# Optimization experiments

Measured on AMD Instinct MI355X. Metric: run time of the kernel, lower is better.

Reference implementation:

```python
import jax, jax.numpy as jnp
import numpy as np

B, S, DIM = 2, 2048, 2048
H = 16
Q_RANK, KV_RANK = 512, 512
D_NOPE, D_ROPE, D_V = 128, 64, 128
D_QK = D_NOPE + D_ROPE  # 192
EPS = 1e-6
SCALE = D_QK ** -0.5


def setup_inputs() -> dict:
    key = jax.random.key(0)
    ks = jax.random.split(key, 8)
    x = jax.random.normal(ks[0], (B, S, DIM), dtype=jnp.float32)
    # real RoPE table: theta_i = 10000^{-2i/d}, angles = pos * theta
    inv_freq = 1.0 / (10000.0 ** (np.arange(0, D_ROPE, 2, dtype=np.float32) / D_ROPE))
    ang = np.arange(S, dtype=np.float32)[:, None] * inv_freq[None, :]  # (S, D_ROPE//2)
    freqs_cis = jnp.asarray(np.stack([np.cos(ang), np.sin(ang)], axis=-1))  # (S, 32, 2)
    std = 0.02
    wq_a = jax.random.normal(ks[1], (Q_RANK, DIM), dtype=jnp.float32) * std
    wq_b = jax.random.normal(ks[2], (H * D_QK, Q_RANK), dtype=jnp.float32) * std
    wkv_a = jax.random.normal(ks[3], (KV_RANK + D_ROPE, DIM), dtype=jnp.float32) * std
    wkv_b = jax.random.normal(ks[4], (H * (D_NOPE + D_V), KV_RANK), dtype=jnp.float32) * std
    wo = jax.random.normal(ks[5], (DIM, H * D_V), dtype=jnp.float32) * std
    q_norm_w = jnp.ones((Q_RANK,), dtype=jnp.float32)
    kv_norm_w = jnp.ones((KV_RANK,), dtype=jnp.float32)
    return {"x": x, "freqs_cis": freqs_cis, "wq_a": wq_a, "wq_b": wq_b,
            "q_norm_w": q_norm_w, "wkv_a": wkv_a, "kv_norm_w": kv_norm_w,
            "wkv_b": wkv_b, "wo": wo}


def _rmsnorm(x, w):
    var = jnp.mean(jnp.square(x), axis=-1, keepdims=True)
    return x * jax.lax.rsqrt(var + EPS) * w


def _rope(x, freqs_cis):
    # x: (B, S, h, d); freqs_cis: (S, d//2, 2) as (cos, sin). Pairs are interleaved (x0,x1),(x2,x3),...
    xr, xi = x[..., 0::2], x[..., 1::2]
    cos = freqs_cis[None, :, None, :, 0]
    sin = freqs_cis[None, :, None, :, 1]
    yr = xr * cos - xi * sin
    yi = xr * sin + xi * cos
    return jnp.stack([yr, yi], axis=-1).reshape(x.shape)


def reference(x, freqs_cis, wq_a, wq_b, q_norm_w, wkv_a, kv_norm_w, wkv_b, wo):
    b, s, _ = x.shape
    # low-rank Q projection: wq_a -> RMSNorm -> wq_b
    q = _rmsnorm(x @ wq_a.T, q_norm_w) @ wq_b.T
    q = q.reshape(b, s, H, D_QK)
    q_nope, q_pe = q[..., :D_NOPE], q[..., D_NOPE:]
    q = jnp.concatenate([q_nope, _rope(q_pe, freqs_cis)], axis=-1)  # (b,s,H,192)
    # KV path
    kv = x @ wkv_a.T  # (b,s,KV_RANK+D_ROPE)
    kv_lat, k_pe = kv[..., :KV_RANK], kv[..., KV_RANK:]
    k_pe = _rope(k_pe[:, :, None, :], freqs_cis)  # (b,s,1,64)
    kv = (_rmsnorm(kv_lat, kv_norm_w) @ wkv_b.T).reshape(b, s, H, D_NOPE + D_V)
    k_nope, v = kv[..., :D_NOPE], kv[..., D_NOPE:]
    k = jnp.concatenate([k_nope, jnp.broadcast_to(k_pe, (b, s, H, D_ROPE))], axis=-1)
    # causal scaled-dot-product attention
    scores = jnp.einsum('bshd,bthd->bhst', q, k) * SCALE
    mask = jnp.tril(jnp.ones((s, s), dtype=bool))
    scores = jnp.where(mask[None, None], scores, jnp.finfo(scores.dtype).min)
    probs = jax.nn.softmax(scores, axis=-1)
    out = jnp.einsum('bhst,bthd->bshd', probs, v).reshape(b, s, H * D_V)
    return out @ wo.T
```

## Files before the change

### kernel.cpp

```cpp
#include <hip/hip_runtime.h>
#include <cstdint>
#include <cstddef>


typedef unsigned short u16;
typedef unsigned int u32;
typedef unsigned long long u64;
typedef __attribute__((ext_vector_type(8))) short bf16x8;
typedef __attribute__((ext_vector_type(4))) float floatx4;

#define MFMA16x16x32 __builtin_amdgcn_mfma_f32_16x16x32_bf16

#define QSCALE 0.10411755f
#define THR_L2 11.541560f

__device__ __forceinline__ u16 f2bf(float f) {
  u32 u = __float_as_uint(f);
  u32 r = (u + 0x7fffu + ((u >> 16) & 1u)) >> 16;
  return (u16)r;
}

__device__ __forceinline__ u32 cvtpk(float lo, float hi) {
  u32 r;
  asm("v_cvt_pk_bf16_f32 %0, %1, %2" : "=v"(r) : "v"(lo), "v"(hi));
  return r;
}

__device__ __forceinline__ void gload16(const void* g, void* l) {
  __builtin_amdgcn_global_load_lds(
      (const __attribute__((address_space(1))) void*)g,
      (__attribute__((address_space(3))) void*)l, 16, 0, 0);
}

__global__ __launch_bounds__(256) void cvt_all(
    const float* __restrict__ s0, const float* __restrict__ s1,
    const float* __restrict__ s2, const float* __restrict__ s3,
    const float* __restrict__ s4, const float* __restrict__ s5,
    u16* __restrict__ d0, u16* __restrict__ d1, u16* __restrict__ d2,
    u16* __restrict__ d3, u16* __restrict__ d4, u16* __restrict__ d5) {
  constexpr int ST1 = 2097152;
  constexpr int ST2 = ST1 + 262144;
  constexpr int ST3 = ST2 + 294912;
  constexpr int ST4 = ST3 + 393216;
  constexpr int ST5 = ST4 + 524288;
  constexpr int TOT = ST5 + 1048576;
  int i = blockIdx.x * 256 + threadIdx.x;
  int stride = gridDim.x * 256;
  for (; i < TOT; i += stride) {
    const float* sp;
    u16* dp;
    int j;
    if (i < ST1)      { sp = s0; dp = d0; j = i; }
    else if (i < ST2) { sp = s1; dp = d1; j = i - ST1; }
    else if (i < ST3) { sp = s2; dp = d2; j = i - ST2; }
    else if (i < ST4) { sp = s3; dp = d3; j = i - ST3; }
    else if (i < ST5) { sp = s4; dp = d4; j = i - ST4; }
    else              { sp = s5; dp = d5; j = i - ST5; }
    float4 v = ((const float4*)sp)[j];
    ushort4 o;
    o.x = f2bf(v.x); o.y = f2bf(v.y); o.z = f2bf(v.z); o.w = f2bf(v.w);
    ((ushort4*)dp)[j] = o;
  }
}

template <int BN>
__global__ __launch_bounds__(256) void gemm_bt(const u16* __restrict__ A,
                                               const u16* __restrict__ B,
                                               float* __restrict__ C,
                                               int M, int N, int K) {
  constexpr int FN = BN / 32;
  constexpr int BL = BN / 64;
  __shared__ alignas(16) u16 As[2][128 * 32];
  __shared__ alignas(16) u16 Bs[2][BN * 32];
  const int m0 = blockIdx.y * 128, n0 = blockIdx.x * BN;
  const int t = threadIdx.x;
  const int wv = t >> 6, lane = t & 63, g = lane >> 4, qq = lane & 15;
  const int wr = wv >> 1, wc = wv & 1;
  const int fsw = (qq >> 1) & 3;
  size_t aoff[2], boff[BL];
#pragma unroll
  for (int i = 0; i < 2; ++i) {
    int seg = t + i * 256;
    int row = seg >> 2, sl = seg & 3;
    aoff[i] = (size_t)(m0 + row) * K + (sl ^ ((row >> 1) & 3)) * 8;
  }
#pragma unroll
  for (int i = 0; i < BL; ++i) {
    int seg = t + i * 256;
    int row = seg >> 2, sl = seg & 3;
    boff[i] = (size_t)(n0 + row) * K + (sl ^ ((row >> 1) & 3)) * 8;
  }
  const floatx4 fz = {0.f, 0.f, 0.f, 0.f};
  floatx4 acc[4][FN];
#pragma unroll
  for (int m = 0; m < 4; ++m)
#pragma unroll
    for (int n = 0; n < FN; ++n) acc[m][n] = fz;

#define GSTAGE(buf, k0)                                                      \
  {                                                                          \
    _Pragma("unroll") for (int i = 0; i < 2; ++i)                            \
        gload16(&A[aoff[i] + (k0)], &As[buf][(size_t)(wv * 64 + i * 256) * 8]); \
    _Pragma("unroll") for (int i = 0; i < BL; ++i)                           \
        gload16(&B[boff[i] + (k0)], &Bs[buf][(size_t)(wv * 64 + i * 256) * 8]); \
  }

  const int nk = K >> 5;
  GSTAGE(0, 0);
  for (int kt = 0; kt < nk; ++kt) {
    asm volatile("" ::: "memory");
    if (kt + 1 < nk) {
      GSTAGE((kt + 1) & 1, (kt + 1) * 32);
      if constexpr (BN == 128)
        asm volatile("s_waitcnt vmcnt(4)" ::: "memory");
      else
        asm volatile("s_waitcnt vmcnt(3)" ::: "memory");
    } else {
      asm volatile("s_waitcnt vmcnt(0)" ::: "memory");
    }
    __builtin_amdgcn_s_barrier();
    asm volatile("" ::: "memory");
    const u16* Ab = &As[kt & 1][0];
    const u16* Bb = &Bs[kt & 1][0];
    bf16x8 af[4], bfr[FN];
#pragma unroll
    for (int m = 0; m < 4; ++m)
      af[m] = *(const bf16x8*)&Ab[(wr * 64 + m * 16 + qq) * 32 + ((g ^ fsw) * 8)];
#pragma unroll
    for (int n = 0; n < FN; ++n)
      bfr[n] = *(const bf16x8*)&Bb[(wc * (BN / 2) + n * 16 + qq) * 32 + ((g ^ fsw) * 8)];
    __builtin_amdgcn_s_setprio(1);
#pragma unroll
    for (int m = 0; m < 4; ++m)
#pragma unroll
      for (int n = 0; n < FN; ++n)
        acc[m][n] = MFMA16x16x32(af[m], bfr[n], acc[m][n], 0, 0, 0);
    __builtin_amdgcn_s_setprio(0);
    asm volatile("" ::: "memory");
    __builtin_amdgcn_s_barrier();
  }
#undef GSTAGE
#pragma unroll
  for (int m = 0; m < 4; ++m)
#pragma unroll
    for (int n = 0; n < FN; ++n)
#pragma unroll
      for (int r = 0; r < 4; ++r) {
        int row = m0 + wr * 64 + m * 16 + 4 * g + r;
        int col = n0 + wc * (BN / 2) + n * 16 + qq;
        C[(size_t)row * N + col] = acc[m][n][r];
      }
}

__global__ __launch_bounds__(256) void rmsnorm_bf16(const float* __restrict__ in,
                                                    int stride,
                                                    const float* __restrict__ w,
                                                    u16* __restrict__ out) {
  const int row = blockIdx.x, t = threadIdx.x;
  __shared__ float wsum[4];
  float2 v = *(const float2*)&in[(size_t)row * stride + 2 * t];
  float ss = v.x * v.x + v.y * v.y;
#pragma unroll
  for (int off = 1; off < 64; off <<= 1) ss += __shfl_xor(ss, off);
  if ((t & 63) == 0) wsum[t >> 6] = ss;
  __syncthreads();
  float tot = wsum[0] + wsum[1] + wsum[2] + wsum[3];
  float r = rsqrtf(tot * (1.f / 512.f) + 1e-6f);
  out[(size_t)row * 512 + 2 * t] = f2bf(v.x * r * w[2 * t]);
  out[(size_t)row * 512 + 2 * t + 1] = f2bf(v.y * r * w[2 * t + 1]);
}

__global__ __launch_bounds__(256) void rope_kpe(const float* __restrict__ ap,
                                                const float* __restrict__ fc,
                                                u16* __restrict__ kpe) {
  int idx = blockIdx.x * 256 + threadIdx.x;
  int row = idx >> 5, j = idx & 31;
  int s = row & 2047;
  float xr = ap[(size_t)row * 1088 + 1024 + 2 * j];
  float xi = ap[(size_t)row * 1088 + 1024 + 2 * j + 1];
  float c = fc[(s * 32 + j) * 2], sn = fc[(s * 32 + j) * 2 + 1];
  u32 lo = f2bf(xr * c - xi * sn), hi = f2bf(xr * sn + xi * c);
  *(u32*)&kpe[(size_t)row * 64 + 2 * j] = lo | (hi << 16);
}

__global__ __launch_bounds__(256) void rope_pack_q(const float* __restrict__ qf,
                                                   const float* __restrict__ fc,
                                                   u16* __restrict__ qbf) {
  int idx = blockIdx.x * 256 + threadIdx.x;
  int j = idx % 96;
  int rh = idx / 96;
  int h = rh & 15, row = rh >> 4;
  int b = row >> 11, s = row & 2047;
  const float* src = qf + (size_t)row * 3072 + h * 192;
  u16* dst = qbf + ((size_t)(b * 16 + h) * 2048 + s) * 192;
  if (j < 64) {
    u32 lo = f2bf(src[2 * j] * QSCALE), hi = f2bf(src[2 * j + 1] * QSCALE);
    *(u32*)&dst[2 * j] = lo | (hi << 16);
  } else {
    int jp = j - 64;
    float xr = src[128 + 2 * jp], xi = src[128 + 2 * jp + 1];
    float c = fc[(s * 32 + jp) * 2], sn = fc[(s * 32 + jp) * 2 + 1];
    u32 lo = f2bf((xr * c - xi * sn) * QSCALE);
    u32 hi = f2bf((xr * sn + xi * c) * QSCALE);
    *(u32*)&dst[128 + 2 * jp] = lo | (hi << 16);
  }
}

__global__ __launch_bounds__(256) void pack_k(const float* __restrict__ kvb,
                                              const u16* __restrict__ kpe,
                                              u16* __restrict__ kbf) {
  int idx = blockIdx.x * 256 + threadIdx.x;
  int j = idx % 96;
  int rh = idx / 96;
  int h = rh & 15, row = rh >> 4;
  int b = row >> 11, s = row & 2047;
  u16* dst = kbf + ((size_t)(b * 16 + h) * 2048 + s) * 192;
  if (j < 64) {
    const float* src = kvb + (size_t)row * 4096 + h * 256;
    u32 lo = f2bf(src[2 * j]), hi = f2bf(src[2 * j + 1]);
    *(u32*)&dst[2 * j] = lo | (hi << 16);
  } else {
    int jp = j - 64;
    *(u32*)&dst[128 + 2 * jp] = *(const u32*)&kpe[(size_t)row * 64 + 2 * jp];
  }
}

__global__ __launch_bounds__(256) void transpose_v(const float* __restrict__ kvb,
                                                   u16* __restrict__ vt) {
  __shared__ u16 T[32][34];
  const int bh = blockIdx.z, b = bh >> 4, h = bh & 15;
  const int s0 = blockIdx.x * 32, d0 = blockIdx.y * 32;
  const int tx = threadIdx.x & 31, ty = threadIdx.x >> 5;
#pragma unroll
  for (int i = 0; i < 4; ++i) {
    int sl = ty + i * 8;
    float v = kvb[(size_t)(b * 2048 + s0 + sl) * 4096 + h * 256 + 128 + d0 + tx];
    T[sl][tx] = f2bf(v);
  }
  __syncthreads();
#pragma unroll
  for (int i = 0; i < 4; ++i) {
    int dl = ty + i * 8;
    vt[((size_t)bh * 128 + d0 + dl) * 2048 + s0 + tx] = T[tx][dl];
  }
}

__global__ __launch_bounds__(256, 4) void flash_attn(const u16* __restrict__ Q,
                                                     const u16* __restrict__ Kc,
                                                     const u16* __restrict__ VT,
                                                     u16* __restrict__ O) {
  __shared__ alignas(16) u16 Ks[2][32 * 192];
  __shared__ alignas(16) u16 Vs[2][128 * 32];
  const int bid = blockIdx.x;
  const int qt = 31 - (bid >> 5);
  const int bh = bid & 31;
  const int t = threadIdx.x, wv = t >> 6, lane = t & 63;
  const int g = lane >> 4, qq = lane & 15;
  const int qrow0 = qt * 64 + wv * 16;
  const int my_last = qrow0 + 15;
  const int q_glob = qrow0 + qq;
  const int nkt = 2 * qt + 2;

  int koffg[3], voffg[2];
#pragma unroll
  for (int i = 0; i < 3; ++i) {
    int seg = t + i * 256;
    int row = seg / 24, sl = seg - row * 24;
    koffg[i] = row * 192 + (sl ^ ((row >> 1) & 7)) * 8;
  }
#pragma unroll
  for (int i = 0; i < 2; ++i) {
    int seg = t + i * 256;
    int row = seg >> 2, sl = seg & 3;
    voffg[i] = row * 2048 + (sl ^ ((row >> 1) & 3)) * 8;
  }
  const u16* Kt0 = Kc + (size_t)bh * 2048 * 192;
  const u16* Vt0 = VT + (size_t)bh * 128 * 2048;

  bf16x8 qf[6];
  {
    const u16* qp = Q + ((size_t)bh * 2048 + qrow0 + qq) * 192;
#pragma unroll
    for (int kk = 0; kk < 6; ++kk) qf[kk] = *(const bf16x8*)&qp[kk * 32 + g * 8];
  }
  asm volatile("s_waitcnt vmcnt(0)" ::: "memory");

  const floatx4 fz = {0.f, 0.f, 0.f, 0.f};
  floatx4 oacc[8];
  floatx4 oacc_l = fz;
#pragma unroll
  for (int d = 0; d < 8; ++d) oacc[d] = fz;
  float m_run = -1e30f;

  bf16x8 ones;
#pragma unroll
  for (int i = 0; i < 8; ++i) ones[i] = (short)0x3f80;

  const int krow0 = 2 * qq;
  const int krow1 = 2 * qq + 1;
  const int xrk = qq & 7;
  const int vsw = (qq >> 1) & 3;

#define STAGE(buf, kt)                                                       \
  {                                                                          \
    const u16* Kg = Kt0 + (size_t)(kt) * (32 * 192);                         \
    const u16* Vg = Vt0 + (kt) * 32;                                         \
    _Pragma("unroll") for (int i = 0; i < 3; ++i)                            \
        gload16(Kg + koffg[i], &Ks[buf][(size_t)(wv * 64 + i * 256) * 8]);   \
    _Pragma("unroll") for (int i = 0; i < 2; ++i)                            \
        gload16(Vg + voffg[i], &Vs[buf][(size_t)(wv * 64 + i * 256) * 8]);   \
  }

  STAGE(0, 0);
  for (int kt = 0; kt < nkt; ++kt) {
    const int k0 = kt * 32;
    asm volatile("" ::: "memory");
    if (kt + 1 < nkt) {
      STAGE((kt + 1) & 1, kt + 1);
      asm volatile("s_waitcnt vmcnt(5)" ::: "memory");
    } else {
      asm volatile("s_waitcnt vmcnt(0)" ::: "memory");
    }
    __builtin_amdgcn_s_barrier();
    asm volatile("" ::: "memory");
    if (k0 <= my_last) {
      const u16* Kb = &Ks[kt & 1][0];
      const u16* Vb = &Vs[kt & 1][0];
      floatx4 s0 = fz, s1 = fz;
      __builtin_amdgcn_s_setprio(1);
#pragma unroll
      for (int kk = 0; kk < 6; ++kk) {
        int sl = kk * 4 + g;
        bf16x8 a0 = *(const bf16x8*)&Kb[krow0 * 192 + ((sl ^ xrk) * 8)];
        bf16x8 a1 = *(const bf16x8*)&Kb[krow1 * 192 + ((sl ^ xrk) * 8)];
        s0 = MFMA16x16x32(a0, qf[kk], s0, 0, 0, 0);
        s1 = MFMA16x16x32(a1, qf[kk], s1, 0, 0, 0);
      }
      __builtin_amdgcn_s_setprio(0);
      float v[8];
      if (k0 + 31 <= qrow0) {
#pragma unroll
        for (int r = 0; r < 4; ++r) {
          v[r] = s0[r];
          v[4 + r] = s1[r];
        }
      } else {
#pragma unroll
        for (int r = 0; r < 4; ++r) {
          int key0 = k0 + 8 * g + 2 * r;
          v[r] = (key0 <= q_glob) ? s0[r] : -1e30f;
          v[4 + r] = (key0 + 1 <= q_glob) ? s1[r] : -1e30f;
        }
      }
      float mloc = fmaxf(fmaxf(fmaxf(v[0], v[1]), fmaxf(v[2], v[3])),
                         fmaxf(fmaxf(v[4], v[5]), fmaxf(v[6], v[7])));
      if (!__all(mloc <= m_run + THR_L2)) {
        float mx = fmaxf(mloc, __shfl_xor(mloc, 16));
        mx = fmaxf(mx, __shfl_xor(mx, 32));
        float m_new = fmaxf(m_run, mx);
        float alpha = exp2f(m_run - m_new);
        m_run = m_new;
#pragma unroll
        for (int d = 0; d < 8; ++d)
#pragma unroll
          for (int r = 0; r < 4; ++r) oacc[d][r] *= alpha;
#pragma unroll
        for (int r = 0; r < 4; ++r) oacc_l[r] *= alpha;
      }
      float pex[8];
#pragma unroll
      for (int i = 0; i < 8; ++i) pex[i] = exp2f(v[i] - m_run);
      bf16x8 pf;
      ((u32*)&pf)[0] = cvtpk(pex[0], pex[4]);
      ((u32*)&pf)[1] = cvtpk(pex[1], pex[5]);
      ((u32*)&pf)[2] = cvtpk(pex[2], pex[6]);
      ((u32*)&pf)[3] = cvtpk(pex[3], pex[7]);
      __builtin_amdgcn_s_setprio(1);
#pragma unroll
      for (int d = 0; d < 8; ++d) {
        bf16x8 vf = *(const bf16x8*)&Vb[(d * 16 + qq) * 32 + ((g ^ vsw) * 8)];
        oacc[d] = MFMA16x16x32(vf, pf, oacc[d], 0, 0, 0);
      }
      oacc_l = MFMA16x16x32(ones, pf, oacc_l, 0, 0, 0);
      __builtin_amdgcn_s_setprio(0);
    }
    asm volatile("" ::: "memory");
    __builtin_amdgcn_s_barrier();
  }
#undef STAGE
  float linv = 1.f / oacc_l[0];
  const int b = bh >> 4, h = bh & 15;
  size_t rowoff = ((size_t)b * 2048 + qrow0 + qq) * 2048 + h * 128 + 4 * g;
#pragma unroll
  for (int d = 0; d < 8; ++d) {
    u32 lo = cvtpk(oacc[d][0] * linv, oacc[d][1] * linv);
    u32 hi = cvtpk(oacc[d][2] * linv, oacc[d][3] * linv);
    u64 w = (u64)lo | ((u64)hi << 32);
    *(u64*)&O[rowoff + d * 16] = w;
  }
}

extern "C" void kernel_launch(void* const* d_in, const int* in_sizes, int n_in,
                              void* d_out, int out_size, void* d_ws,
                              size_t ws_size, hipStream_t stream) {
  (void)in_sizes; (void)n_in; (void)out_size;
  const float* x = (const float*)d_in[0];
  const float* fc = (const float*)d_in[1];
  const float* wqa = (const float*)d_in[2];
  const float* wqb = (const float*)d_in[3];
  const float* qnw = (const float*)d_in[4];
  const float* wkva = (const float*)d_in[5];
  const float* kvnw = (const float*)d_in[6];
  const float* wkvb = (const float*)d_in[7];
  const float* wo = (const float*)d_in[8];
  float* out = (float*)d_out;
  char* ws = (char*)d_ws;

  size_t off = 0;
  auto alloc = [&](size_t bytes) {
    size_t o = off;
    off += (bytes + 255) & ~(size_t)255;
    return o;
  };
  const size_t o_xbf = alloc(16777216);
  const size_t o_wa = alloc(4456448);
  const size_t o_wqb = alloc(3145728);
  const size_t o_wkvb = alloc(4194304);
  const size_t o_wo = alloc(8388608);
  const size_t o_qln = alloc(4194304);
  const size_t o_kvln = alloc(4194304);
  const size_t o_kpe = alloc(524288);
  const size_t o_big = alloc(67108864);
  const size_t o_qbf = alloc(25165824);
  const size_t o_kbf = alloc(25165824);
  const size_t o_vt = alloc(16777216);
  if (ws_size < off) return;

  u16* xbf = (u16*)(ws + o_xbf);
  u16* wab = (u16*)(ws + o_wa);
  u16* wqbb = (u16*)(ws + o_wqb);
  u16* wkvbb = (u16*)(ws + o_wkvb);
  u16* wob = (u16*)(ws + o_wo);
  u16* qlatn = (u16*)(ws + o_qln);
  u16* kvlatn = (u16*)(ws + o_kvln);
  u16* kpe = (u16*)(ws + o_kpe);
  float* aproj = (float*)(ws + o_big);
  float* qfull = (float*)(ws + o_big);
  float* kvb = (float*)(ws + o_big);
  u16* qbf = (u16*)(ws + o_qbf);
  u16* kbf = (u16*)(ws + o_kbf);
  u16* vt = (u16*)(ws + o_vt);
  u16* attnbf = (u16*)(ws + o_xbf);

  cvt_all<<<2048, 256, 0, stream>>>(x, wqa, wkva, wqb, wkvb, wo,
                                    xbf, wab, wab + 1048576, wqbb, wkvbb, wob);

  gemm_bt<64><<<dim3(17, 32), 256, 0, stream>>>(xbf, wab, aproj, 4096, 1088, 2048);
  rmsnorm_bf16<<<4096, 256, 0, stream>>>(aproj, 1088, qnw, qlatn);
  rmsnorm_bf16<<<4096, 256, 0, stream>>>(aproj + 512, 1088, kvnw, kvlatn);
  rope_kpe<<<512, 256, 0, stream>>>(aproj, fc, kpe);

  gemm_bt<128><<<dim3(24, 32), 256, 0, stream>>>(qlatn, wqbb, qfull, 4096, 3072, 512);
  rope_pack_q<<<24576, 256, 0, stream>>>(qfull, fc, qbf);

  gemm_bt<128><<<dim3(32, 32), 256, 0, stream>>>(kvlatn, wkvbb, kvb, 4096, 4096, 512);
  pack_k<<<24576, 256, 0, stream>>>(kvb, kpe, kbf);
  transpose_v<<<dim3(64, 4, 32), 256, 0, stream>>>(kvb, vt);

  flash_attn<<<1024, 256, 0, stream>>>(qbf, kbf, vt, attnbf);
  gemm_bt<128><<<dim3(16, 32), 256, 0, stream>>>(attnbf, wob, out, 4096, 2048, 2048);
}
```

Measured before the change: 289.3 us.

## Replace GEMMs with 8-wave large-tile kernel and emit bf16 intermediates

Adds a templated 512-thread GEMM with 128x256 or 256x256 tiles. It keeps two K-stages in flight and reissues the next load right after the LDS fragment reads, instead of waiting for a trailing barrier. The Q and KV up-projection GEMMs now write bf16 directly, so the downstream rope, pack and transpose kernels read half the bytes and skip their own conversion. The first projection's N is padded from 1088 to 1280 to fit the tile. The padded weight rows are never written and the extra columns are wasted compute. The larger tiles give fewer blocks than there are CUs for some GEMMs.

```diff
diff --git a/kernel.cpp b/kernel.cpp
--- a/kernel.cpp
+++ b/kernel.cpp
@@ -19,13 +19,14 @@
   u32 r = (u + 0x7fffu + ((u >> 16) & 1u)) >> 16;
   return (u16)r;
 }
-
+__device__ __forceinline__ float bf2f(u16 b) {
+  return __uint_as_float(((u32)b) << 16);
+}
 __device__ __forceinline__ u32 cvtpk(float lo, float hi) {
   u32 r;
   asm("v_cvt_pk_bf16_f32 %0, %1, %2" : "=v"(r) : "v"(lo), "v"(hi));
   return r;
 }
-
 __device__ __forceinline__ void gload16(const void* g, void* l) {
   __builtin_amdgcn_global_load_lds(
       (const __attribute__((address_space(1))) void*)g,
@@ -63,55 +64,58 @@
   }
 }
 
-template <int BN>
-__global__ __launch_bounds__(256) void gemm_bt(const u16* __restrict__ A,
-                                               const u16* __restrict__ B,
-                                               float* __restrict__ C,
-                                               int M, int N, int K) {
-  constexpr int FN = BN / 32;
-  constexpr int BL = BN / 64;
-  __shared__ alignas(16) u16 As[2][128 * 32];
+template <int BM, int BN, bool OBF16>
+__global__ __launch_bounds__(512) void gemm8(const u16* __restrict__ A,
+                                             const u16* __restrict__ B,
+                                             void* __restrict__ Cv,
+                                             int M, int N, int K) {
+  constexpr int WM = BM / 2;
+  constexpr int AF = WM / 16;
+  constexpr int LA = BM * 4 / 512;
+  constexpr int LB = BN * 4 / 512;
+  constexpr int S = LA + LB;
+  __shared__ alignas(16) u16 As[2][BM * 32];
   __shared__ alignas(16) u16 Bs[2][BN * 32];
-  const int m0 = blockIdx.y * 128, n0 = blockIdx.x * BN;
+  const int m0 = blockIdx.y * BM, n0 = blockIdx.x * BN;
   const int t = threadIdx.x;
   const int wv = t >> 6, lane = t & 63, g = lane >> 4, qq = lane & 15;
-  const int wr = wv >> 1, wc = wv & 1;
+  const int wr = wv >> 2, wc = wv & 3;
   const int fsw = (qq >> 1) & 3;
-  size_t aoff[2], boff[BL];
-#pragma unroll
-  for (int i = 0; i < 2; ++i) {
-    int seg = t + i * 256;
+  size_t aoff[LA], boff[LB];
+#pragma unroll
+  for (int i = 0; i < LA; ++i) {
+    int seg = t + i * 512;
     int row = seg >> 2, sl = seg & 3;
     aoff[i] = (size_t)(m0 + row) * K + (sl ^ ((row >> 1) & 3)) * 8;
   }
 #pragma unroll
-  for (int i = 0; i < BL; ++i) {
-    int seg = t + i * 256;
+  for (int i = 0; i < LB; ++i) {
+    int seg = t + i * 512;
     int row = seg >> 2, sl = seg & 3;
     boff[i] = (size_t)(n0 + row) * K + (sl ^ ((row >> 1) & 3)) * 8;
   }
   const floatx4 fz = {0.f, 0.f, 0.f, 0.f};
-  floatx4 acc[4][FN];
-#pragma unroll
-  for (int m = 0; m < 4; ++m)
-#pragma unroll
-    for (int n = 0; n < FN; ++n) acc[m][n] = fz;
-
-#define GSTAGE(buf, k0)                                                      \
-  {                                                                          \
-    _Pragma("unroll") for (int i = 0; i < 2; ++i)                            \
-        gload16(&A[aoff[i] + (k0)], &As[buf][(size_t)(wv * 64 + i * 256) * 8]); \
-    _Pragma("unroll") for (int i = 0; i < BL; ++i)                           \
-        gload16(&B[boff[i] + (k0)], &Bs[buf][(size_t)(wv * 64 + i * 256) * 8]); \
+  floatx4 acc[AF][4];
+#pragma unroll
+  for (int m = 0; m < AF; ++m)
+#pragma unroll
+    for (int n = 0; n < 4; ++n) acc[m][n] = fz;
+
+#define GS8(buf, k0)                                                          \
+  {                                                                           \
+    _Pragma("unroll") for (int i = 0; i < LA; ++i)                            \
+        gload16(&A[aoff[i] + (k0)], &As[buf][(size_t)(wv * 64 + i * 512) * 8]); \
+    _Pragma("unroll") for (int i = 0; i < LB; ++i)                            \
+        gload16(&B[boff[i] + (k0)], &Bs[buf][(size_t)(wv * 64 + i * 512) * 8]); \
   }
 
   const int nk = K >> 5;
-  GSTAGE(0, 0);
+  GS8(0, 0);
+  GS8(1, 32);
   for (int kt = 0; kt < nk; ++kt) {
     asm volatile("" ::: "memory");
     if (kt + 1 < nk) {
-      GSTAGE((kt + 1) & 1, (kt + 1) * 32);
-      if constexpr (BN == 128)
+      if constexpr (S == 4)
         asm volatile("s_waitcnt vmcnt(4)" ::: "memory");
       else
         asm volatile("s_waitcnt vmcnt(3)" ::: "memory");
@@ -122,33 +126,38 @@
     asm volatile("" ::: "memory");
     const u16* Ab = &As[kt & 1][0];
     const u16* Bb = &Bs[kt & 1][0];
-    bf16x8 af[4], bfr[FN];
-#pragma unroll
-    for (int m = 0; m < 4; ++m)
-      af[m] = *(const bf16x8*)&Ab[(wr * 64 + m * 16 + qq) * 32 + ((g ^ fsw) * 8)];
-#pragma unroll
-    for (int n = 0; n < FN; ++n)
-      bfr[n] = *(const bf16x8*)&Bb[(wc * (BN / 2) + n * 16 + qq) * 32 + ((g ^ fsw) * 8)];
+    bf16x8 af[AF], bfr[4];
+#pragma unroll
+    for (int m = 0; m < AF; ++m)
+      af[m] = *(const bf16x8*)&Ab[(wr * WM + m * 16 + qq) * 32 + ((g ^ fsw) * 8)];
+#pragma unroll
+    for (int n = 0; n < 4; ++n)
+      bfr[n] = *(const bf16x8*)&Bb[(wc * 64 + n * 16 + qq) * 32 + ((g ^ fsw) * 8)];
+    asm volatile("s_waitcnt lgkmcnt(0)" ::: "memory");
+    __builtin_amdgcn_s_barrier();
+    asm volatile("" ::: "memory");
+    if (kt + 2 < nk) GS8(kt & 1, (kt + 2) * 32);
     __builtin_amdgcn_s_setprio(1);
 #pragma unroll
-    for (int m = 0; m < 4; ++m)
-#pragma unroll
-      for (int n = 0; n < FN; ++n)
+    for (int m = 0; m < AF; ++m)
+#pragma unroll
+      for (int n = 0; n < 4; ++n)
         acc[m][n] = MFMA16x16x32(af[m], bfr[n], acc[m][n], 0, 0, 0);
     __builtin_amdgcn_s_setprio(0);
-    asm volatile("" ::: "memory");
-    __builtin_amdgcn_s_barrier();
-  }
-#undef GSTAGE
-#pragma unroll
-  for (int m = 0; m < 4; ++m)
-#pragma unroll
-    for (int n = 0; n < FN; ++n)
+  }
+#undef GS8
+#pragma unroll
+  for (int m = 0; m < AF; ++m)
+#pragma unroll
+    for (int n = 0; n < 4; ++n)
 #pragma unroll
       for (int r = 0; r < 4; ++r) {
-        int row = m0 + wr * 64 + m * 16 + 4 * g + r;
-        int col = n0 + wc * (BN / 2) + n * 16 + qq;
-        C[(size_t)row * N + col] = acc[m][n][r];
+        int row = m0 + wr * WM + m * 16 + 4 * g + r;
+        int col = n0 + wc * 64 + n * 16 + qq;
+        if constexpr (OBF16)
+          ((u16*)Cv)[(size_t)row * N + col] = f2bf(acc[m][n][r]);
+        else
+          ((float*)Cv)[(size_t)row * N + col] = acc[m][n][r];
       }
 }
 
@@ -176,14 +185,14 @@
   int idx = blockIdx.x * 256 + threadIdx.x;
   int row = idx >> 5, j = idx & 31;
   int s = row & 2047;
-  float xr = ap[(size_t)row * 1088 + 1024 + 2 * j];
-  float xi = ap[(size_t)row * 1088 + 1024 + 2 * j + 1];
+  float xr = ap[(size_t)row * 1280 + 1024 + 2 * j];
+  float xi = ap[(size_t)row * 1280 + 1024 + 2 * j + 1];
   float c = fc[(s * 32 + j) * 2], sn = fc[(s * 32 + j) * 2 + 1];
   u32 lo = f2bf(xr * c - xi * sn), hi = f2bf(xr * sn + xi * c);
   *(u32*)&kpe[(size_t)row * 64 + 2 * j] = lo | (hi << 16);
 }
 
-__global__ __launch_bounds__(256) void rope_pack_q(const float* __restrict__ qf,
+__global__ __launch_bounds__(256) void rope_pack_q(const u16* __restrict__ qf,
                                                    const float* __restrict__ fc,
                                                    u16* __restrict__ qbf) {
   int idx = blockIdx.x * 256 + threadIdx.x;
@@ -191,14 +200,17 @@
   int rh = idx / 96;
   int h = rh & 15, row = rh >> 4;
   int b = row >> 11, s = row & 2047;
-  const float* src = qf + (size_t)row * 3072 + h * 192;
+  const u16* src = qf + (size_t)row * 3072 + h * 192;
   u16* dst = qbf + ((size_t)(b * 16 + h) * 2048 + s) * 192;
   if (j < 64) {
-    u32 lo = f2bf(src[2 * j] * QSCALE), hi = f2bf(src[2 * j + 1] * QSCALE);
+    u32 w = *(const u32*)&src[2 * j];
+    u32 lo = f2bf(bf2f((u16)w) * QSCALE);
+    u32 hi = f2bf(bf2f((u16)(w >> 16)) * QSCALE);
     *(u32*)&dst[2 * j] = lo | (hi << 16);
   } else {
     int jp = j - 64;
-    float xr = src[128 + 2 * jp], xi = src[128 + 2 * jp + 1];
+    u32 w = *(const u32*)&src[128 + 2 * jp];
+    float xr = bf2f((u16)w), xi = bf2f((u16)(w >> 16));
     float c = fc[(s * 32 + jp) * 2], sn = fc[(s * 32 + jp) * 2 + 1];
     u32 lo = f2bf((xr * c - xi * sn) * QSCALE);
     u32 hi = f2bf((xr * sn + xi * c) * QSCALE);
@@ -206,7 +218,7 @@
   }
 }
 
-__global__ __launch_bounds__(256) void pack_k(const float* __restrict__ kvb,
+__global__ __launch_bounds__(256) void pack_k(const u16* __restrict__ kvb,
                                               const u16* __restrict__ kpe,
                                               u16* __restrict__ kbf) {
   int idx = blockIdx.x * 256 + threadIdx.x;
@@ -216,16 +228,14 @@
   int b = row >> 11, s = row & 2047;
   u16* dst = kbf + ((size_t)(b * 16 + h) * 2048 + s) * 192;
   if (j < 64) {
-    const float* src = kvb + (size_t)row * 4096 + h * 256;
-    u32 lo = f2bf(src[2 * j]), hi = f2bf(src[2 * j + 1]);
-    *(u32*)&dst[2 * j] = lo | (hi << 16);
+    *(u32*)&dst[2 * j] = *(const u32*)&kvb[(size_t)row * 4096 + h * 256 + 2 * j];
   } else {
     int jp = j - 64;
     *(u32*)&dst[128 + 2 * jp] = *(const u32*)&kpe[(size_t)row * 64 + 2 * jp];
   }
 }
 
-__global__ __launch_bounds__(256) void transpose_v(const float* __restrict__ kvb,
+__global__ __launch_bounds__(256) void transpose_v(const u16* __restrict__ kvb,
                                                    u16* __restrict__ vt) {
   __shared__ u16 T[32][34];
   const int bh = blockIdx.z, b = bh >> 4, h = bh & 15;
@@ -234,8 +244,7 @@
 #pragma unroll
   for (int i = 0; i < 4; ++i) {
     int sl = ty + i * 8;
-    float v = kvb[(size_t)(b * 2048 + s0 + sl) * 4096 + h * 256 + 128 + d0 + tx];
-    T[sl][tx] = f2bf(v);
+    T[sl][tx] = kvb[(size_t)(b * 2048 + s0 + sl) * 4096 + h * 256 + 128 + d0 + tx];
   }
   __syncthreads();
 #pragma unroll
@@ -423,14 +432,14 @@
     return o;
   };
   const size_t o_xbf = alloc(16777216);
-  const size_t o_wa = alloc(4456448);
+  const size_t o_wa = alloc(5242880);
   const size_t o_wqb = alloc(3145728);
   const size_t o_wkvb = alloc(4194304);
   const size_t o_wo = alloc(8388608);
   const size_t o_qln = alloc(4194304);
   const size_t o_kvln = alloc(4194304);
   const size_t o_kpe = alloc(524288);
-  const size_t o_big = alloc(67108864);
+  const size_t o_big = alloc(33554432);
   const size_t o_qbf = alloc(25165824);
   const size_t o_kbf = alloc(25165824);
   const size_t o_vt = alloc(16777216);
@@ -445,8 +454,8 @@
   u16* kvlatn = (u16*)(ws + o_kvln);
   u16* kpe = (u16*)(ws + o_kpe);
   float* aproj = (float*)(ws + o_big);
-  float* qfull = (float*)(ws + o_big);
-  float* kvb = (float*)(ws + o_big);
+  u16* qfb = (u16*)(ws + o_big);
+  u16* kvbb = (u16*)(ws + o_big);
   u16* qbf = (u16*)(ws + o_qbf);
   u16* kbf = (u16*)(ws + o_kbf);
   u16* vt = (u16*)(ws + o_vt);
@@ -455,18 +464,22 @@
   cvt_all<<<2048, 256, 0, stream>>>(x, wqa, wkva, wqb, wkvb, wo,
                                     xbf, wab, wab + 1048576, wqbb, wkvbb, wob);
 
-  gemm_bt<64><<<dim3(17, 32), 256, 0, stream>>>(xbf, wab, aproj, 4096, 1088, 2048);
-  rmsnorm_bf16<<<4096, 256, 0, stream>>>(aproj, 1088, qnw, qlatn);
-  rmsnorm_bf16<<<4096, 256, 0, stream>>>(aproj + 512, 1088, kvnw, kvlatn);
+  gemm8<128, 256, false><<<dim3(5, 32), 512, 0, stream>>>(
+      xbf, wab, aproj, 4096, 1280, 2048);
+  rmsnorm_bf16<<<4096, 256, 0, stream>>>(aproj, 1280, qnw, qlatn);
+  rmsnorm_bf16<<<4096, 256, 0, stream>>>(aproj + 512, 1280, kvnw, kvlatn);
   rope_kpe<<<512, 256, 0, stream>>>(aproj, fc, kpe);
 
-  gemm_bt<128><<<dim3(24, 32), 256, 0, stream>>>(qlatn, wqbb, qfull, 4096, 3072, 512);
-  rope_pack_q<<<24576, 256, 0, stream>>>(qfull, fc, qbf);
-
-  gemm_bt<128><<<dim3(32, 32), 256, 0, stream>>>(kvlatn, wkvbb, kvb, 4096, 4096, 512);
-  pack_k<<<24576, 256, 0, stream>>>(kvb, kpe, kbf);
-  transpose_v<<<dim3(64, 4, 32), 256, 0, stream>>>(kvb, vt);
+  gemm8<256, 256, true><<<dim3(12, 16), 512, 0, stream>>>(
+      qlatn, wqbb, qfb, 4096, 3072, 512);
+  rope_pack_q<<<24576, 256, 0, stream>>>(qfb, fc, qbf);
+
+  gemm8<256, 256, true><<<dim3(16, 16), 512, 0, stream>>>(
+      kvlatn, wkvbb, kvbb, 4096, 4096, 512);
+  pack_k<<<24576, 256, 0, stream>>>(kvbb, kpe, kbf);
+  transpose_v<<<dim3(64, 4, 32), 256, 0, stream>>>(kvbb, vt);
 
   flash_attn<<<1024, 256, 0, stream>>>(qbf, kbf, vt, attnbf);
-  gemm_bt<128><<<dim3(16, 32), 256, 0, stream>>>(attnbf, wob, out, 4096, 2048, 2048);
-}
+  gemm8<128, 256, false><<<dim3(8, 32), 512, 0, stream>>>(
+      attnbf, wob, out, 4096, 2048, 2048);
+}
```

After: 289.5 us. Within noise of the previous version (+0.0%).
